# Optimization experiments

Hardware: AMD Instinct MI355X
Metric: run time of the kernel (lower is better)

Reference implementation:

```python
import jax, jax.numpy as jnp
import numpy as np

N_NODES = 10000
N_EDGES = 160000


def setup_inputs() -> dict:
    key = jax.random.key(0)
    ks = jax.random.split(key, 12)
    B, N, DIN, DH, DOUT, L = 8, N_NODES, 512, 256, 3, 6
    s = lambda *d: 1.0 / np.sqrt(d[-2])
    return {
        "x": jax.random.normal(ks[0], (B, N, DIN), jnp.float32),
        "edge_src": jax.random.randint(ks[1], (N_EDGES,), 0, N, jnp.int32),
        "edge_dst": jax.random.randint(ks[2], (N_EDGES,), 0, N, jnp.int32),
        "edge_w": jax.random.uniform(ks[3], (N_EDGES,), jnp.float32) / 16.0,  # ~row-normalized
        "W_in": jax.random.normal(ks[4], (DIN, DH), jnp.float32) * s(DIN, DH),
        "LW_in": jax.random.normal(ks[5], (DIN, DH), jnp.float32) * s(DIN, DH),
        "b_in": jnp.zeros((DH,), jnp.float32),
        "W_blk": jax.random.normal(ks[6], (L, 2, DH, DH), jnp.float32) * s(DH, DH),
        "LW_blk": jax.random.normal(ks[7], (L, 2, DH, DH), jnp.float32) * s(DH, DH),
        "b_blk": jnp.zeros((L, 2, DH), jnp.float32),
        "W_out": jax.random.normal(ks[8], (DH, DOUT), jnp.float32) * s(DH, DOUT),
        "LW_out": jax.random.normal(ks[9], (DH, DOUT), jnp.float32) * s(DH, DOUT),
        "b_out": jnp.zeros((DOUT,), jnp.float32),
    }


def _gconv(x, esrc, edst, ew, W, LW, b):
    # x: [B,N,Din] -> [B,N,Dout]; out = A @ (x W) + x LW + b with sparse A
    support = jnp.einsum("bnd,de->bne", x, W)
    msgs = support[:, esrc, :] * ew[None, :, None]          # [B,E,Do]
    agg = jax.ops.segment_sum(msgs.transpose(1, 0, 2), edst,
                              num_segments=x.shape[1])       # [N,B,Do]
    agg = agg.transpose(1, 0, 2)                             # [B,N,Do]
    return agg + jnp.einsum("bnd,de->bne", x, LW) + b


def reference(x, edge_src, edge_dst, edge_w, W_in, LW_in, b_in,
              W_blk, LW_blk, b_blk, W_out, LW_out, b_out):
    h = _gconv(x, edge_src, edge_dst, edge_w, W_in, LW_in, b_in)
    for l in range(W_blk.shape[0]):  # GResBlock: two GConvs, residual, *0.5
        t = _gconv(h, edge_src, edge_dst, edge_w, W_blk[l, 0], LW_blk[l, 0], b_blk[l, 0])
        t = _gconv(t, edge_src, edge_dst, edge_w, W_blk[l, 1], LW_blk[l, 1], b_blk[l, 1])
        h = (h + t) * 0.5
    x_out = _gconv(h, edge_src, edge_dst, edge_w, W_out, LW_out, b_out)
    return (x_out, h)
```

## Files before the change

### kernel.cpp

```cpp
#include <hip/hip_runtime.h>

#define NN 10000
#define BB 8
#define MROWS 80000

typedef float f32x4 __attribute__((ext_vector_type(4)));
typedef _Float16 f16;
typedef _Float16 f16x8 __attribute__((ext_vector_type(8)));

typedef __attribute__((address_space(1))) void as1_void;
typedef __attribute__((address_space(3))) void as3_void;

static __device__ __forceinline__ void gl_lds16(const void* g, void* l){
  __builtin_amdgcn_global_load_lds((as1_void*)g, (as3_void*)l, 16, 0, 0);
}

__global__ void k_count(const int* __restrict__ dst, int E, int* __restrict__ counts){
  int i = blockIdx.x * blockDim.x + threadIdx.x;
  if(i < E) atomicAdd(&counts[dst[i]], 1);
}

__global__ void k_scan(const int* __restrict__ counts, int* __restrict__ rp){
  __shared__ int buf[1024];
  __shared__ int carry;
  const int t = threadIdx.x;
  if(t == 0){ carry = 0; rp[0] = 0; }
  __syncthreads();
  for(int base = 0; base < NN; base += 1024){
    int v = (base + t < NN) ? counts[base + t] : 0;
    buf[t] = v;
    __syncthreads();
    for(int off = 1; off < 1024; off <<= 1){
      int x = (t >= off) ? buf[t - off] : 0;
      __syncthreads();
      buf[t] += x;
      __syncthreads();
    }
    if(base + t < NN) rp[base + t + 1] = carry + buf[t];
    __syncthreads();
    if(t == 0) carry += buf[1023];
    __syncthreads();
  }
}

__global__ void k_fill(const int* __restrict__ dst, int E, const int* __restrict__ rp,
                       int* __restrict__ cursor, int* __restrict__ ci){
  int i = blockIdx.x * blockDim.x + threadIdx.x;
  if(i < E){
    int d = dst[i];
    int p = rp[d] + atomicAdd(&cursor[d], 1);
    ci[p] = i;
  }
}

__global__ void k_sort_rows(const int* __restrict__ rp, int* __restrict__ ci, float* __restrict__ vw,
                            const int* __restrict__ esrc, const float* __restrict__ ew){
  const int n = blockIdx.x * blockDim.x + threadIdx.x;
  if(n >= NN) return;
  const int s = rp[n], e = rp[n + 1];
  for(int i = s; i < e - 1; ++i){
    int mj = i, mv = ci[i];
    for(int j = i + 1; j < e; ++j){
      int v = ci[j];
      if(v < mv){ mv = v; mj = j; }
    }
    ci[mj] = ci[i]; ci[i] = mv;
  }
  for(int p = s; p < e; ++p){
    int eid = ci[p];
    ci[p] = esrc[eid];
    vw[p] = ew[eid];
  }
}

__global__ void k_cvt(const float4* __restrict__ in, f16x8* __restrict__ out, int n8){
  int i = blockIdx.x * blockDim.x + threadIdx.x;
  if(i >= n8) return;
  float4 v0 = in[2 * i], v1 = in[2 * i + 1];
  f16x8 o;
  o[0] = (f16)v0.x; o[1] = (f16)v0.y; o[2] = (f16)v0.z; o[3] = (f16)v0.w;
  o[4] = (f16)v1.x; o[5] = (f16)v1.y; o[6] = (f16)v1.z; o[7] = (f16)v1.w;
  out[i] = o;
}

__global__ void k_pack_w(const float* __restrict__ Wi, const float* __restrict__ LWi,
                         const float* __restrict__ Wb, const float* __restrict__ LWb,
                         f16* __restrict__ dh){
  const int T0 = 512 * 512;
  const int TOT = T0 + 12 * 512 * 256;
  int i = blockIdx.x * blockDim.x + threadIdx.x;
  if(i >= TOT) return;
  float v;
  if(i < T0){
    int c = i >> 9, k = i & 511;
    v = (c < 256) ? Wi[k * 256 + c] : LWi[k * 256 + (c - 256)];
  } else {
    int j = i - T0;
    int li = j >> 17;
    int r = j & 131071;
    int c = r >> 8, k = r & 255;
    const float* src = (c < 256) ? (Wb + (size_t)li * 65536) : (LWb + (size_t)li * 65536);
    v = src[k * 256 + (c & 255)];
  }
  dh[i] = (f16)v;
}

__global__ __launch_bounds__(256) void k_gemm_dual(
    const f16* __restrict__ A, const f16* __restrict__ Bt,
    f16* __restrict__ Sup, f16* __restrict__ Loc, int K, int nblk)
{
  __shared__ f16 As[2][2048];
  __shared__ f16 Bs[2][8192];
  const int t = threadIdx.x;
  const int pid = blockIdx.x;
  const int q = nblk >> 3, r = nblk & 7;
  const int xcd = pid & 7, sl = pid >> 3;
  const int wg = (xcd < r ? xcd * (q + 1) : r * (q + 1) + (xcd - r) * q) + sl;
  const int m0 = (wg >> 1) << 6;
  const int by = wg & 1;
  const int n0 = by << 8;
  const int lane = t & 63, wv = t >> 6;
  const int rA = lane & 15, g = lane >> 4;
  f32x4 acc[4][4] = {};
  const int nsteps = K >> 5;
  const int rowt = t >> 2;
  const int csw  = (t & 3) ^ ((rowt >> 1) & 3);
  const int cbt  = csw << 3;

  auto STAGE = [&](int s, int buf){
    const int k0 = s << 5;
    const size_t aoff = (size_t)(m0 + rowt) * K + k0 + cbt;
    gl_lds16(A + aoff, (char*)As[buf] + t * 16);
    #pragma unroll
    for(int qq = 0; qq < 4; ++qq){
      const size_t boff = (size_t)(n0 + qq * 64 + rowt) * K + k0 + cbt;
      gl_lds16(Bt + boff, (char*)Bs[buf] + qq * 4096 + t * 16);
    }
  };

  STAGE(0, 0);
  int cur = 0;
  const int slotx = (rA >> 1) & 3;

  for(int s = 0; s < nsteps; ++s){
    __builtin_amdgcn_sched_barrier(0);
    if(s + 1 < nsteps){
      STAGE(s + 1, cur ^ 1);
      asm volatile("s_waitcnt vmcnt(5)" ::: "memory");
    } else {
      asm volatile("s_waitcnt vmcnt(0)" ::: "memory");
    }
    __builtin_amdgcn_s_barrier();
    __builtin_amdgcn_sched_barrier(0);

    f16x8 av[4], bv[4];
    #pragma unroll
    for(int mi = 0; mi < 4; ++mi){
      const int ao = (mi * 16 + rA) * 32 + ((g ^ slotx) << 3);
      av[mi] = *(const f16x8*)(As[cur] + ao);
    }
    #pragma unroll
    for(int ni = 0; ni < 4; ++ni){
      const int bo = wv * 2048 + (ni * 16 + rA) * 32 + ((g ^ slotx) << 3);
      bv[ni] = *(const f16x8*)(Bs[cur] + bo);
    }
    #pragma unroll
    for(int mi = 0; mi < 4; ++mi){
      #pragma unroll
      for(int ni = 0; ni < 4; ++ni){
        acc[mi][ni] = __builtin_amdgcn_mfma_f32_16x16x32_f16(av[mi], bv[ni], acc[mi][ni], 0, 0, 0);
      }
    }
    __builtin_amdgcn_sched_barrier(0);
    __builtin_amdgcn_s_barrier();
    cur ^= 1;
  }

  f16* dst = (by == 0) ? Sup : Loc;
  const int wn = wv << 6;
  #pragma unroll
  for(int mi = 0; mi < 4; ++mi){
    const int rowb = m0 + mi * 16 + g * 4;
    #pragma unroll
    for(int ni = 0; ni < 4; ++ni){
      const int col = wn + ni * 16 + rA;
      #pragma unroll
      for(int r2 = 0; r2 < 4; ++r2){
        dst[(size_t)(rowb + r2) * 256 + col] = (f16)acc[mi][ni][r2];
      }
    }
  }
}

__global__ __launch_bounds__(256) void k_agg(
    const f16* __restrict__ Sup, const f16* __restrict__ Loc,
    const float* __restrict__ bias,
    const int* __restrict__ rp, const int* __restrict__ ci, const float* __restrict__ vw,
    const f16* __restrict__ Hprev, f16* __restrict__ Hnext,
    float* __restrict__ hout, const int mode)
{
  const int pid = blockIdx.x;
  const int half = (pid >= 5000) ? 1 : 0;
  const int rem = pid - half * 5000;
  const int b = rem & 7;
  const int grp = rem >> 3;
  const int t = threadIdx.x;
  const int j = t >> 4;
  const int tt = t & 15;
  const int n = grp * 16 + j;
  const int d0 = half * 128 + tt * 8;
  const size_t rowbase = ((size_t)b * NN + n) * 256 + d0;
  float a[8];
  {
    const f16x8 lv = *(const f16x8*)(Loc + rowbase);
    float4 q0 = *(const float4*)(bias + d0);
    float4 q1 = *(const float4*)(bias + d0 + 4);
    a[0] = (float)lv[0] + q0.x; a[1] = (float)lv[1] + q0.y;
    a[2] = (float)lv[2] + q0.z; a[3] = (float)lv[3] + q0.w;
    a[4] = (float)lv[4] + q1.x; a[5] = (float)lv[5] + q1.y;
    a[6] = (float)lv[6] + q1.z; a[7] = (float)lv[7] + q1.w;
  }
  const int s = rp[n], e = rp[n + 1];
  const size_t bb = (size_t)b * NN * 256 + d0;
  for(int i = s; i < e; ++i){
    const int src = ci[i];
    const float w = vw[i];
    const f16x8 sv = *(const f16x8*)(Sup + bb + (size_t)src * 256);
    a[0] = fmaf(w, (float)sv[0], a[0]);
    a[1] = fmaf(w, (float)sv[1], a[1]);
    a[2] = fmaf(w, (float)sv[2], a[2]);
    a[3] = fmaf(w, (float)sv[3], a[3]);
    a[4] = fmaf(w, (float)sv[4], a[4]);
    a[5] = fmaf(w, (float)sv[5], a[5]);
    a[6] = fmaf(w, (float)sv[6], a[6]);
    a[7] = fmaf(w, (float)sv[7], a[7]);
  }
  if(mode >= 2){
    const f16x8 hp = *(const f16x8*)(Hprev + rowbase);
    #pragma unroll
    for(int k = 0; k < 8; ++k) a[k] = (a[k] + (float)hp[k]) * 0.5f;
  }
  if(mode == 3){
    *(float4*)(hout + rowbase)     = make_float4(a[0], a[1], a[2], a[3]);
    *(float4*)(hout + rowbase + 4) = make_float4(a[4], a[5], a[6], a[7]);
    return;
  }
  f16x8 o;
  #pragma unroll
  for(int k = 0; k < 8; ++k) o[k] = (f16)a[k];
  *(f16x8*)(Hnext + rowbase) = o;
}

__global__ __launch_bounds__(256) void k_out_sup(const float* __restrict__ h,
    const float* __restrict__ Wo, float* __restrict__ sup3){
  const int gid = blockIdx.x * 4 + (threadIdx.x >> 6);
  const int lane = threadIdx.x & 63;
  if(gid >= MROWS) return;
  const float4 v = *(const float4*)(h + (size_t)gid * 256 + lane * 4);
  const float hv[4] = {v.x, v.y, v.z, v.w};
  float p0 = 0.f, p1 = 0.f, p2 = 0.f;
  #pragma unroll
  for(int j = 0; j < 4; ++j){
    const int k = lane * 4 + j;
    p0 = fmaf(hv[j], Wo[k * 3 + 0], p0);
    p1 = fmaf(hv[j], Wo[k * 3 + 1], p1);
    p2 = fmaf(hv[j], Wo[k * 3 + 2], p2);
  }
  #pragma unroll
  for(int off = 32; off; off >>= 1){
    p0 += __shfl_xor(p0, off, 64);
    p1 += __shfl_xor(p1, off, 64);
    p2 += __shfl_xor(p2, off, 64);
  }
  if(lane == 0){
    float* o = sup3 + (size_t)gid * 3;
    o[0] = p0; o[1] = p1; o[2] = p2;
  }
}

__global__ __launch_bounds__(256) void k_out_final(const float* __restrict__ h,
    const float* __restrict__ LWo, const float* __restrict__ bo,
    const int* __restrict__ rp, const int* __restrict__ ci, const float* __restrict__ vw,
    const float* __restrict__ sup3, float* __restrict__ out){
  const int gid = blockIdx.x * 4 + (threadIdx.x >> 6);
  const int lane = threadIdx.x & 63;
  if(gid >= MROWS) return;
  const int b = gid / NN, n = gid % NN;
  const float4 v = *(const float4*)(h + (size_t)gid * 256 + lane * 4);
  const float hv[4] = {v.x, v.y, v.z, v.w};
  float p0 = 0.f, p1 = 0.f, p2 = 0.f;
  #pragma unroll
  for(int j = 0; j < 4; ++j){
    const int k = lane * 4 + j;
    p0 = fmaf(hv[j], LWo[k * 3 + 0], p0);
    p1 = fmaf(hv[j], LWo[k * 3 + 1], p1);
    p2 = fmaf(hv[j], LWo[k * 3 + 2], p2);
  }
  const int s = rp[n], e = rp[n + 1];
  for(int i = s + lane; i < e; i += 64){
    const int src = ci[i];
    const float w = vw[i];
    const float* sp = sup3 + ((size_t)b * NN + src) * 3;
    p0 = fmaf(w, sp[0], p0);
    p1 = fmaf(w, sp[1], p1);
    p2 = fmaf(w, sp[2], p2);
  }
  #pragma unroll
  for(int off = 32; off; off >>= 1){
    p0 += __shfl_xor(p0, off, 64);
    p1 += __shfl_xor(p1, off, 64);
    p2 += __shfl_xor(p2, off, 64);
  }
  if(lane == 0){
    float* o = out + (size_t)gid * 3;
    o[0] = p0 + bo[0]; o[1] = p1 + bo[1]; o[2] = p2 + bo[2];
  }
}

extern "C" void kernel_launch(void* const* d_in, const int* in_sizes, int n_in,
                              void* d_out, int out_size, void* d_ws, size_t ws_size,
                              hipStream_t stream) {
  const float* x     = (const float*)d_in[0];
  const int*   esrc  = (const int*)d_in[1];
  const int*   edst  = (const int*)d_in[2];
  const float* ew    = (const float*)d_in[3];
  const float* W_in  = (const float*)d_in[4];
  const float* LW_in = (const float*)d_in[5];
  const float* b_in  = (const float*)d_in[6];
  const float* W_blk = (const float*)d_in[7];
  const float* LW_blk= (const float*)d_in[8];
  const float* b_blk = (const float*)d_in[9];
  const float* W_out = (const float*)d_in[10];
  const float* LW_out= (const float*)d_in[11];
  const float* b_out = (const float*)d_in[12];
  const int E = in_sizes[1];

  float* outF  = (float*)d_out;
  float* xout  = outF;
  float* hOut  = outF + 240000;
  f16* x16 = (f16*)hOut;

  char* ws = (char*)d_ws;
  size_t off = 0;
  auto alloc = [&](size_t bytes) -> char* {
    char* p = ws + off;
    off += (bytes + 255) & ~(size_t)255;
    return p;
  };
  const size_t HB = (size_t)20480000 * 2;
  f16* Ha  = (f16*)alloc(HB);
  f16* Hb  = (f16*)alloc(HB);
  f16* Sup = (f16*)alloc(HB);
  f16* Loc = (f16*)alloc(HB);
  const int WTOT = 512 * 512 + 12 * 512 * 256;
  f16* Wt = (f16*)alloc((size_t)WTOT * 2);
  float* sup3    = (float*)alloc((size_t)240000 * 4);
  int*   counts  = (int*)alloc((size_t)2 * NN * 4);
  int*   cursor  = counts + NN;
  int*   rp      = (int*)alloc((size_t)(NN + 1) * 4);
  int*   ci      = (int*)alloc((size_t)E * 4);
  float* vw      = (float*)alloc((size_t)E * 4);
  (void)ws_size; (void)n_in; (void)out_size;

  hipMemsetAsync(counts, 0, (size_t)2 * NN * 4, stream);
  k_count<<<(E + 255) / 256, 256, 0, stream>>>(edst, E, counts);
  k_scan<<<1, 1024, 0, stream>>>(counts, rp);
  k_fill<<<(E + 255) / 256, 256, 0, stream>>>(edst, E, rp, cursor, ci);
  k_sort_rows<<<(NN + 255) / 256, 256, 0, stream>>>(rp, ci, vw, esrc, ew);

  k_cvt<<<(5120000 + 255) / 256, 256, 0, stream>>>((const float4*)x, (f16x8*)x16, 5120000);
  k_pack_w<<<(WTOT + 255) / 256, 256, 0, stream>>>(W_in, LW_in, W_blk, LW_blk, Wt);

  const int NBLK = 2500;
  const int ABLK = 10000;
  k_gemm_dual<<<NBLK, 256, 0, stream>>>(x16, Wt, Sup, Loc, 512, NBLK);
  k_agg<<<ABLK, 256, 0, stream>>>(Sup, Loc, b_in, rp, ci, vw, Ha, Ha, xout, 0);

  const f16* Wm = Wt + 512 * 512;
  for(int l = 0; l < 6; ++l){
    const int li0 = 2 * l, li1 = 2 * l + 1;
    k_gemm_dual<<<NBLK, 256, 0, stream>>>(Ha, Wm + (size_t)li0 * 131072, Sup, Loc, 256, NBLK);
    k_agg<<<ABLK, 256, 0, stream>>>(Sup, Loc, b_blk + li0 * 256, rp, ci, vw, Ha, Hb, xout, 0);
    k_gemm_dual<<<NBLK, 256, 0, stream>>>(Hb, Wm + (size_t)li1 * 131072, Sup, Loc, 256, NBLK);
    k_agg<<<ABLK, 256, 0, stream>>>(Sup, Loc, b_blk + li1 * 256, rp, ci, vw, Ha, Ha, hOut, (l == 5) ? 3 : 2);
  }

  k_out_sup<<<MROWS / 4, 256, 0, stream>>>(hOut, W_out, sup3);
  k_out_final<<<MROWS / 4, 256, 0, stream>>>(hOut, LW_out, b_out, rp, ci, vw, sup3, xout);
}
```

Before: 1.743 ms.

## Stage column-sliced support panels in LDS for sparse aggregation with padded CSR

```diff
diff --git a/kernel.cpp b/kernel.cpp
--- a/kernel.cpp
+++ b/kernel.cpp
@@ -5,7 +5,9 @@
 #define MROWS 80000
 
 typedef float f32x4 __attribute__((ext_vector_type(4)));
+typedef unsigned int u32x4 __attribute__((ext_vector_type(4)));
 typedef _Float16 f16;
+typedef _Float16 f16x4 __attribute__((ext_vector_type(4)));
 typedef _Float16 f16x8 __attribute__((ext_vector_type(8)));
 
 typedef __attribute__((address_space(1))) void as1_void;
@@ -20,14 +22,14 @@
   if(i < E) atomicAdd(&counts[dst[i]], 1);
 }
 
-__global__ void k_scan(const int* __restrict__ counts, int* __restrict__ rp){
+__global__ void k_scan(const int* __restrict__ counts, int* __restrict__ rp2){
   __shared__ int buf[1024];
   __shared__ int carry;
   const int t = threadIdx.x;
-  if(t == 0){ carry = 0; rp[0] = 0; }
+  if(t == 0){ carry = 0; rp2[0] = 0; }
   __syncthreads();
   for(int base = 0; base < NN; base += 1024){
-    int v = (base + t < NN) ? counts[base + t] : 0;
+    int v = (base + t < NN) ? ((counts[base + t] + 1) & ~1) : 0;
     buf[t] = v;
     __syncthreads();
     for(int off = 1; off < 1024; off <<= 1){
@@ -36,28 +38,31 @@
       buf[t] += x;
       __syncthreads();
     }
-    if(base + t < NN) rp[base + t + 1] = carry + buf[t];
+    if(base + t < NN) rp2[base + t + 1] = carry + buf[t];
     __syncthreads();
     if(t == 0) carry += buf[1023];
     __syncthreads();
   }
 }
 
-__global__ void k_fill(const int* __restrict__ dst, int E, const int* __restrict__ rp,
+__global__ void k_fill(const int* __restrict__ dst, int E, const int* __restrict__ rp2,
                        int* __restrict__ cursor, int* __restrict__ ci){
   int i = blockIdx.x * blockDim.x + threadIdx.x;
   if(i < E){
     int d = dst[i];
-    int p = rp[d] + atomicAdd(&cursor[d], 1);
+    int p = rp2[d] + atomicAdd(&cursor[d], 1);
     ci[p] = i;
   }
 }
 
-__global__ void k_sort_rows(const int* __restrict__ rp, int* __restrict__ ci, float* __restrict__ vw,
+__global__ void k_sort_rows(const int* __restrict__ rp2, const int* __restrict__ cursor,
+                            int* __restrict__ ci, unsigned int* __restrict__ ev,
                             const int* __restrict__ esrc, const float* __restrict__ ew){
   const int n = blockIdx.x * blockDim.x + threadIdx.x;
   if(n >= NN) return;
-  const int s = rp[n], e = rp[n + 1];
+  const int s = rp2[n];
+  const int deg = cursor[n];
+  const int e = s + deg;
   for(int i = s; i < e - 1; ++i){
     int mj = i, mv = ci[i];
     for(int j = i + 1; j < e; ++j){
@@ -68,8 +73,13 @@
   }
   for(int p = s; p < e; ++p){
     int eid = ci[p];
-    ci[p] = esrc[eid];
-    vw[p] = ew[eid];
+    ev[2 * p]     = (unsigned int)esrc[eid];
+    ev[2 * p + 1] = __float_as_uint(ew[eid]);
+  }
+  const int e2 = rp2[n + 1];
+  for(int p = e; p < e2; ++p){
+    ev[2 * p]     = 0u;
+    ev[2 * p + 1] = 0u;
   }
 }
 
@@ -107,7 +117,7 @@
 
 __global__ __launch_bounds__(256) void k_gemm_dual(
     const f16* __restrict__ A, const f16* __restrict__ Bt,
-    f16* __restrict__ Sup, f16* __restrict__ Loc, int K, int nblk)
+    f16* __restrict__ SupBlk, f16* __restrict__ Loc, int K, int nblk)
 {
   __shared__ f16 As[2][2048];
   __shared__ f16 Bs[2][8192];
@@ -176,79 +186,97 @@
     cur ^= 1;
   }
 
-  f16* dst = (by == 0) ? Sup : Loc;
   const int wn = wv << 6;
-  #pragma unroll
-  for(int mi = 0; mi < 4; ++mi){
-    const int rowb = m0 + mi * 16 + g * 4;
-    #pragma unroll
-    for(int ni = 0; ni < 4; ++ni){
-      const int col = wn + ni * 16 + rA;
+  if(by == 0){
+    #pragma unroll
+    for(int mi = 0; mi < 4; ++mi){
+      const int rowb = m0 + mi * 16 + g * 4;
       #pragma unroll
       for(int r2 = 0; r2 < 4; ++r2){
-        dst[(size_t)(rowb + r2) * 256 + col] = (f16)acc[mi][ni][r2];
+        const int row = rowb + r2;
+        const int bb2 = row / 10000;
+        const int nn2 = row - bb2 * 10000;
+        #pragma unroll
+        for(int ni = 0; ni < 4; ++ni){
+          const int col = wn + ni * 16 + rA;
+          SupBlk[((size_t)((bb2 << 6) + (col >> 2)) * 10000 + nn2) * 4 + (col & 3)] = (f16)acc[mi][ni][r2];
+        }
       }
     }
-  }
-}
-
-__global__ __launch_bounds__(256) void k_agg(
-    const f16* __restrict__ Sup, const f16* __restrict__ Loc,
+  } else {
+    #pragma unroll
+    for(int mi = 0; mi < 4; ++mi){
+      const int rowb = m0 + mi * 16 + g * 4;
+      #pragma unroll
+      for(int ni = 0; ni < 4; ++ni){
+        const int col = wn + ni * 16 + rA;
+        #pragma unroll
+        for(int r2 = 0; r2 < 4; ++r2){
+          Loc[(size_t)(rowb + r2) * 256 + col] = (f16)acc[mi][ni][r2];
+        }
+      }
+    }
+  }
+}
+
+__global__ __launch_bounds__(1024, 8) void k_agg_lds(
+    const f16* __restrict__ SupBlk, const f16* __restrict__ Loc,
     const float* __restrict__ bias,
-    const int* __restrict__ rp, const int* __restrict__ ci, const float* __restrict__ vw,
+    const int* __restrict__ rp2, const unsigned int* __restrict__ ev,
     const f16* __restrict__ Hprev, f16* __restrict__ Hnext,
     float* __restrict__ hout, const int mode)
 {
+  __shared__ f16 panel[40000];
   const int pid = blockIdx.x;
-  const int half = (pid >= 5000) ? 1 : 0;
-  const int rem = pid - half * 5000;
-  const int b = rem & 7;
-  const int grp = rem >> 3;
+  const int b = pid & 7;
+  const int slice = pid >> 3;
+  const int ds = slice << 2;
   const int t = threadIdx.x;
-  const int j = t >> 4;
-  const int tt = t & 15;
-  const int n = grp * 16 + j;
-  const int d0 = half * 128 + tt * 8;
-  const size_t rowbase = ((size_t)b * NN + n) * 256 + d0;
-  float a[8];
-  {
-    const f16x8 lv = *(const f16x8*)(Loc + rowbase);
-    float4 q0 = *(const float4*)(bias + d0);
-    float4 q1 = *(const float4*)(bias + d0 + 4);
-    a[0] = (float)lv[0] + q0.x; a[1] = (float)lv[1] + q0.y;
-    a[2] = (float)lv[2] + q0.z; a[3] = (float)lv[3] + q0.w;
-    a[4] = (float)lv[4] + q1.x; a[5] = (float)lv[5] + q1.y;
-    a[6] = (float)lv[6] + q1.z; a[7] = (float)lv[7] + q1.w;
-  }
-  const int s = rp[n], e = rp[n + 1];
-  const size_t bb = (size_t)b * NN * 256 + d0;
-  for(int i = s; i < e; ++i){
-    const int src = ci[i];
-    const float w = vw[i];
-    const f16x8 sv = *(const f16x8*)(Sup + bb + (size_t)src * 256);
-    a[0] = fmaf(w, (float)sv[0], a[0]);
-    a[1] = fmaf(w, (float)sv[1], a[1]);
-    a[2] = fmaf(w, (float)sv[2], a[2]);
-    a[3] = fmaf(w, (float)sv[3], a[3]);
-    a[4] = fmaf(w, (float)sv[4], a[4]);
-    a[5] = fmaf(w, (float)sv[5], a[5]);
-    a[6] = fmaf(w, (float)sv[6], a[6]);
-    a[7] = fmaf(w, (float)sv[7], a[7]);
-  }
-  if(mode >= 2){
-    const f16x8 hp = *(const f16x8*)(Hprev + rowbase);
-    #pragma unroll
-    for(int k = 0; k < 8; ++k) a[k] = (a[k] + (float)hp[k]) * 0.5f;
-  }
-  if(mode == 3){
-    *(float4*)(hout + rowbase)     = make_float4(a[0], a[1], a[2], a[3]);
-    *(float4*)(hout + rowbase + 4) = make_float4(a[4], a[5], a[6], a[7]);
-    return;
-  }
-  f16x8 o;
-  #pragma unroll
-  for(int k = 0; k < 8; ++k) o[k] = (f16)a[k];
-  *(f16x8*)(Hnext + rowbase) = o;
+
+  const f16* psrc = SupBlk + (size_t)((b << 6) + slice) * 40000;
+  for(int c = t; c < 5000; c += 1024)
+    gl_lds16(psrc + c * 8, (char*)panel + c * 16);
+  asm volatile("s_waitcnt vmcnt(0)" ::: "memory");
+  __syncthreads();
+
+  const float4 bz = *(const float4*)(bias + ds);
+  for(int k = 0; k < 10; ++k){
+    const int n = t + (k << 10);
+    if(n >= NN) continue;
+    const int s = rp2[n], e = rp2[n + 1];
+    const size_t rb = ((size_t)b * NN + n) * 256 + ds;
+    const f16x4 lv = *(const f16x4*)(Loc + rb);
+    float a0 = (float)lv[0] + bz.x;
+    float a1 = (float)lv[1] + bz.y;
+    float a2 = (float)lv[2] + bz.z;
+    float a3 = (float)lv[3] + bz.w;
+    for(int i = s; i < e; i += 2){
+      const u32x4 ee = *(const u32x4*)(ev + 2 * i);
+      const int s0 = (int)ee[0]; const float w0 = __uint_as_float(ee[1]);
+      const int s1 = (int)ee[2]; const float w1 = __uint_as_float(ee[3]);
+      const f16x4 h0 = *(const f16x4*)(panel + s0 * 4);
+      const f16x4 h1 = *(const f16x4*)(panel + s1 * 4);
+      a0 = fmaf(w0, (float)h0[0], a0); a0 = fmaf(w1, (float)h1[0], a0);
+      a1 = fmaf(w0, (float)h0[1], a1); a1 = fmaf(w1, (float)h1[1], a1);
+      a2 = fmaf(w0, (float)h0[2], a2); a2 = fmaf(w1, (float)h1[2], a2);
+      a3 = fmaf(w0, (float)h0[3], a3); a3 = fmaf(w1, (float)h1[3], a3);
+    }
+    if(mode >= 2){
+      const f16x4 hp = *(const f16x4*)(Hprev + rb);
+      a0 = (a0 + (float)hp[0]) * 0.5f;
+      a1 = (a1 + (float)hp[1]) * 0.5f;
+      a2 = (a2 + (float)hp[2]) * 0.5f;
+      a3 = (a3 + (float)hp[3]) * 0.5f;
+    }
+    if(mode == 3){
+      f32x4 o = {a0, a1, a2, a3};
+      *(f32x4*)(hout + rb) = o;
+    } else {
+      f16x4 o;
+      o[0] = (f16)a0; o[1] = (f16)a1; o[2] = (f16)a2; o[3] = (f16)a3;
+      *(f16x4*)(Hnext + rb) = o;
+    }
+  }
 }
 
 __global__ __launch_bounds__(256) void k_out_sup(const float* __restrict__ h,
@@ -280,7 +308,7 @@
 
 __global__ __launch_bounds__(256) void k_out_final(const float* __restrict__ h,
     const float* __restrict__ LWo, const float* __restrict__ bo,
-    const int* __restrict__ rp, const int* __restrict__ ci, const float* __restrict__ vw,
+    const int* __restrict__ rp2, const unsigned int* __restrict__ ev,
     const float* __restrict__ sup3, float* __restrict__ out){
   const int gid = blockIdx.x * 4 + (threadIdx.x >> 6);
   const int lane = threadIdx.x & 63;
@@ -296,10 +324,10 @@
     p1 = fmaf(hv[j], LWo[k * 3 + 1], p1);
     p2 = fmaf(hv[j], LWo[k * 3 + 2], p2);
   }
-  const int s = rp[n], e = rp[n + 1];
+  const int s = rp2[n], e = rp2[n + 1];
   for(int i = s + lane; i < e; i += 64){
-    const int src = ci[i];
-    const float w = vw[i];
+    const int src = (int)ev[2 * i];
+    const float w = __uint_as_float(ev[2 * i + 1]);
     const float* sp = sup3 + ((size_t)b * NN + src) * 3;
     p0 = fmaf(w, sp[0], p0);
     p1 = fmaf(w, sp[1], p1);
@@ -357,34 +385,34 @@
   float* sup3    = (float*)alloc((size_t)240000 * 4);
   int*   counts  = (int*)alloc((size_t)2 * NN * 4);
   int*   cursor  = counts + NN;
-  int*   rp      = (int*)alloc((size_t)(NN + 1) * 4);
-  int*   ci      = (int*)alloc((size_t)E * 4);
-  float* vw      = (float*)alloc((size_t)E * 4);
+  int*   rp2     = (int*)alloc((size_t)(NN + 1) * 4);
+  int*   ci      = (int*)alloc((size_t)(E + NN) * 4);
+  unsigned int* ev = (unsigned int*)alloc((size_t)2 * (E + NN) * 4);
   (void)ws_size; (void)n_in; (void)out_size;
 
   hipMemsetAsync(counts, 0, (size_t)2 * NN * 4, stream);
   k_count<<<(E + 255) / 256, 256, 0, stream>>>(edst, E, counts);
-  k_scan<<<1, 1024, 0, stream>>>(counts, rp);
-  k_fill<<<(E + 255) / 256, 256, 0, stream>>>(edst, E, rp, cursor, ci);
-  k_sort_rows<<<(NN + 255) / 256, 256, 0, stream>>>(rp, ci, vw, esrc, ew);
+  k_scan<<<1, 1024, 0, stream>>>(counts, rp2);
+  k_fill<<<(E + 255) / 256, 256, 0, stream>>>(edst, E, rp2, cursor, ci);
+  k_sort_rows<<<(NN + 255) / 256, 256, 0, stream>>>(rp2, cursor, ci, ev, esrc, ew);
 
   k_cvt<<<(5120000 + 255) / 256, 256, 0, stream>>>((const float4*)x, (f16x8*)x16, 5120000);
   k_pack_w<<<(WTOT + 255) / 256, 256, 0, stream>>>(W_in, LW_in, W_blk, LW_blk, Wt);
 
   const int NBLK = 2500;
-  const int ABLK = 10000;
+  const int ABLK = 512;
   k_gemm_dual<<<NBLK, 256, 0, stream>>>(x16, Wt, Sup, Loc, 512, NBLK);
-  k_agg<<<ABLK, 256, 0, stream>>>(Sup, Loc, b_in, rp, ci, vw, Ha, Ha, xout, 0);
+  k_agg_lds<<<ABLK, 1024, 0, stream>>>(Sup, Loc, b_in, rp2, ev, Ha, Ha, xout, 0);
 
   const f16* Wm = Wt + 512 * 512;
   for(int l = 0; l < 6; ++l){
     const int li0 = 2 * l, li1 = 2 * l + 1;
     k_gemm_dual<<<NBLK, 256, 0, stream>>>(Ha, Wm + (size_t)li0 * 131072, Sup, Loc, 256, NBLK);
-    k_agg<<<ABLK, 256, 0, stream>>>(Sup, Loc, b_blk + li0 * 256, rp, ci, vw, Ha, Hb, xout, 0);
+    k_agg_lds<<<ABLK, 1024, 0, stream>>>(Sup, Loc, b_blk + li0 * 256, rp2, ev, Ha, Hb, xout, 0);
     k_gemm_dual<<<NBLK, 256, 0, stream>>>(Hb, Wm + (size_t)li1 * 131072, Sup, Loc, 256, NBLK);
-    k_agg<<<ABLK, 256, 0, stream>>>(Sup, Loc, b_blk + li1 * 256, rp, ci, vw, Ha, Ha, hOut, (l == 5) ? 3 : 2);
+    k_agg_lds<<<ABLK, 1024, 0, stream>>>(Sup, Loc, b_blk + li1 * 256, rp2, ev, Ha, Ha, hOut, (l == 5) ? 3 : 2);
   }
 
   k_out_sup<<<MROWS / 4, 256, 0, stream>>>(hOut, W_out, sup3);
-  k_out_final<<<MROWS / 4, 256, 0, stream>>>(hOut, LW_out, b_out, rp, ci, vw, sup3, xout);
-}
+  k_out_final<<<MROWS / 4, 256, 0, stream>>>(hOut, LW_out, b_out, rp2, ev, sup3, xout);
+}
```

Result: slower. 3.482 ms (+99.8%).
